# Kernel tuning notes

Measured on AMD Instinct MI355X. Metric: run time of the kernel, lower is better.

## Reference

```python
import jax, jax.numpy as jnp
import numpy as np


def setup_inputs() -> dict:
    key = jax.random.key(0)
    k1, k2, k3 = jax.random.split(key, 3)
    B, N, D = 8, 4096, 64
    q = jax.random.normal(k1, (B, N, D), dtype=jnp.float32)
    k = jax.random.normal(k2, (B, N, D), dtype=jnp.float32)
    v = jax.random.normal(k3, (B, N, D), dtype=jnp.float32)
    attn_mask = jnp.ones((B, N), dtype=jnp.int32)  # 1 = attend, 0 = padding
    return {"q": q, "k": k, "v": v, "attn_mask": attn_mask}


def reference(q, k, v, attn_mask):
    # q: [B, n_q, d], k/v: [B, n_k, d], attn_mask: [B, n_k]
    d = q.shape[-1]
    n_q, n_k = q.shape[1], k.shape[1]
    scale = jnp.sqrt(jnp.asarray(d, dtype=q.dtype))
    # [B, n_q, n_k] attention logits
    logits = jnp.einsum("bqd,bkd->bqk", q, k) / scale
    # causal (mask_future=True): tril keep-mask over (n_q, n_k)
    causal = jnp.tril(jnp.ones((n_q, n_k), dtype=bool))
    neg_inf = jnp.asarray(-jnp.inf, dtype=logits.dtype)
    logits = jnp.where(causal[None, :, :], logits, neg_inf)
    # padding mask broadcast over query dim: [B, 1, n_k]
    logits = jnp.where(attn_mask[:, None, :] == 0, neg_inf, logits)
    w = jax.nn.softmax(logits, axis=-1)
    return jnp.einsum("bqk,bkd->bqd", w, v)
```

## Files before the change

kernel.cpp:

```cpp
#include <hip/hip_runtime.h>


#define BATCH 8
#define SEQ   4096
#define DIM   64
#define QT    64
#define NKT   (SEQ / 64)

typedef __attribute__((ext_vector_type(8))) short bf16x8;
typedef __attribute__((ext_vector_type(4))) float f32x4;
typedef __attribute__((ext_vector_type(4))) unsigned u32x4;

__device__ inline short f2bf(float f) {
    unsigned u = __builtin_bit_cast(unsigned, f);
    u += 0x7FFFu + ((u >> 16) & 1u);
    return (short)(u >> 16);
}

__device__ inline unsigned pk2bf(float a, float b) {
    unsigned ua = __builtin_bit_cast(unsigned, a) + 0x8000u;
    unsigned ub = __builtin_bit_cast(unsigned, b) + 0x8000u;
    return __builtin_amdgcn_perm(ub, ua, 0x07060302u);
}

__device__ inline float fast_exp2(float x) {
#if __has_builtin(__builtin_amdgcn_exp2f)
    return __builtin_amdgcn_exp2f(x);
#else
    return exp2f(x);
#endif
}

__device__ inline void gl_lds16(const void* g, void* l) {
    __builtin_amdgcn_global_load_lds(
        (const __attribute__((address_space(1))) void*)g,
        (__attribute__((address_space(3))) void*)l, 16, 0, 0);
}

__global__ __launch_bounds__(256)
void prep_kv(const float* __restrict__ kg, const float* __restrict__ vg,
             const int* __restrict__ mg, short* __restrict__ kw,
             short* __restrict__ vw, float* __restrict__ mf) {
    const int tile = blockIdx.x;
    const float* kp = kg + (size_t)tile * 64 * DIM;
    const float* vp = vg + (size_t)tile * 64 * DIM;
    short* ko = kw + (size_t)tile * 4096;
    short* vo = vw + (size_t)tile * 4096;
    const int t = threadIdx.x;
    if (mf && t < 64) {
        const int* mp = mg + (size_t)tile * 64;
        mf[(size_t)tile * 64 + t] = mp[t] ? 0.0f : -1e30f;
    }
#pragma unroll
    for (int i = 0; i < 4; ++i) {
        const int flat = i * 256 + t;
        const int key = flat >> 4, d0 = (flat & 15) * 4;
        const float4 kv = *(const float4*)(kp + (size_t)key * DIM + d0);
        uint2 kpk;
        kpk.x = pk2bf(kv.x, kv.y); kpk.y = pk2bf(kv.z, kv.w);
        *(uint2*)(ko + (((d0 >> 3) << 6) + key) * 8 + (d0 & 7)) = kpk;
        const float4 vv = *(const float4*)(vp + (size_t)key * DIM + d0);
        const int vcell = ((key >> 5) << 2) | ((key >> 2) & 3);
        const int vj    = (((key >> 4) & 1) << 2) | (key & 3);
        vo[((vcell << 6) + d0 + 0) * 8 + vj] = f2bf(vv.x);
        vo[((vcell << 6) + d0 + 1) * 8 + vj] = f2bf(vv.y);
        vo[((vcell << 6) + d0 + 2) * 8 + vj] = f2bf(vv.z);
        vo[((vcell << 6) + d0 + 3) * 8 + vj] = f2bf(vv.w);
    }
}

__global__ __launch_bounds__(512, 6)
void attn_split3(const float* __restrict__ qg, float* __restrict__ og,
                 const short* __restrict__ kw, const short* __restrict__ vw,
                 const float* __restrict__ mf, float* __restrict__ opart,
                 float* __restrict__ lpart) {
    __shared__ __align__(16) char smem[32768];
    short* KbS = (short*)smem;
    short* VbS = (short*)(smem + 16384);
    float* OX = (float*)smem;
    float* LB = (float*)(smem + 16384);

    const int t    = threadIdx.x;
    const int w    = t >> 6;
    const int L    = t & 63;
    const int c15  = L & 15;
    const int quad = L >> 4;
    const int qsub = w & 3;
    const int kh   = w >> 2;

    const int id  = blockIdx.x;
    const int b   = id & 7;
    const int r_  = id >> 3;
    const int j   = r_ & 31;
    const int ch  = r_ >> 5;
    const int nL  = 64 - j;
    const int qLt = 63 - j;

    const float* qp  = qg + (size_t)b * SEQ * DIM;
    const float* mb  = mf + (size_t)b * SEQ;
    const short* kwb = kw + (size_t)b * NKT * 4096;
    const short* vwb = vw + (size_t)b * NKT * 4096;
    float* osl = opart + (size_t)(b * 32 + j) * 8192;
    float* lsl = lpart + (size_t)(b * 32 + j) * 256;
    const float qscale = 0.125f * 1.44269504088896340736f;

    auto stage = [&](int bs, int kt) {
        const short* ks = kwb + (size_t)kt * 4096;
        const short* vs = vwb + (size_t)kt * 4096;
        const int off = w << 9;
        gl_lds16(ks + off + (L << 3), KbS + bs * 4096 + off);
        gl_lds16(vs + off + (L << 3), VbS + bs * 4096 + off);
    };

    int sqt[2], sk0[2], sk1[2], smode[2], sos[2], sls[2], nseg;
    sos[0] = sos[1] = 0; sls[0] = sls[1] = 0;
    if (ch == 0) {
        nseg = 1;
        sqt[0] = qLt; sk0[0] = 0;  sk1[0] = 22; smode[0] = 0; sls[0] = 0;
    } else if (ch == 1) {
        if (nL >= 44) {
            nseg = 1;
            sqt[0] = qLt; sk0[0] = 22; sk1[0] = 44; smode[0] = 1; sos[0] = 0; sls[0] = 1;
        } else {
            nseg = 2;
            sqt[0] = qLt; sk0[0] = 22; sk1[0] = nL;      smode[0] = 1; sos[0] = 0; sls[0] = 1;
            sqt[1] = j;   sk0[1] = 0;  sk1[1] = 44 - nL; smode[1] = 0; sls[1] = 3;
        }
    } else {
        if (nL > 44) {
            nseg = 2;
            sqt[0] = qLt; sk0[0] = 44; sk1[0] = nL;    smode[0] = 1; sos[0] = 1; sls[0] = 2;
            sqt[1] = j;   sk0[1] = 0;  sk1[1] = j + 1; smode[1] = 2;
        } else if (nL == 44) {
            nseg = 1;
            sqt[0] = j; sk0[0] = 0; sk1[0] = j + 1; smode[0] = 2;
        } else {
            nseg = 1;
            sqt[0] = j; sk0[0] = 44 - nL; sk1[0] = j + 1; smode[0] = 1; sos[0] = 1; sls[0] = 2;
        }
    }

    for (int seg = 0; seg < nseg; ++seg) {
        const int qt   = sqt[seg];
        const int kt0  = sk0[seg];
        const int kt1  = sk1[seg];
        const int mode = smode[seg];

        const int qbase = qt * QT;
        const int qrow  = qbase + qsub * 16 + c15;

        bf16x8 Qf[2];
#pragma unroll
        for (int c = 0; c < 2; ++c) {
            const float* src = qp + (size_t)qrow * DIM + c * 32 + quad * 8;
            float4 x = *(const float4*)(src);
            float4 y = *(const float4*)(src + 4);
            bf16x8 f;
            f[0] = f2bf(x.x * qscale); f[1] = f2bf(x.y * qscale);
            f[2] = f2bf(x.z * qscale); f[3] = f2bf(x.w * qscale);
            f[4] = f2bf(y.x * qscale); f[5] = f2bf(y.y * qscale);
            f[6] = f2bf(y.z * qscale); f[7] = f2bf(y.w * qscale);
            Qf[c] = f;
        }

        float lsum = 0.0f;
        f32x4 Oacc[4];
#pragma unroll
        for (int nb = 0; nb < 4; ++nb) Oacc[nb] = (f32x4){0.f, 0.f, 0.f, 0.f};

        stage(0, kt0);

        for (int kt = kt0; kt < kt1; ++kt) {
            const int cur = (kt - kt0) & 1;
            __syncthreads();
            if (kt + 1 < kt1) stage(cur ^ 1, kt + 1);

            const short* Kt = KbS + cur * 4096;
            const short* Vt = VbS + cur * 4096;

            const float4 ma0 = *(const float4*)&mb[kt * 64 + (2 * kh + 0) * 16 + quad * 4];
            const float4 ma1 = *(const float4*)&mb[kt * 64 + (2 * kh + 1) * 16 + quad * 4];

            f32x4 sacc[2];
            sacc[0] = (f32x4){0.f, 0.f, 0.f, 0.f};
            sacc[1] = (f32x4){0.f, 0.f, 0.f, 0.f};
#pragma unroll
            for (int c = 0; c < 2; ++c) {
#pragma unroll
                for (int i = 0; i < 2; ++i) {
                    bf16x8 kf = *(const bf16x8*)&Kt[(((quad + 4 * c) << 6) + (2 * kh + i) * 16 + c15) * 8];
                    sacc[i] = __builtin_amdgcn_mfma_f32_16x16x32_bf16(kf, Qf[c], sacc[i], 0, 0, 0);
                }
            }

            const bool diag = (kt == qt);
            unsigned pu[4];
#pragma unroll
            for (int i = 0; i < 2; ++i) {
                const int kb = 2 * kh + i;
                const float4 ma = i ? ma1 : ma0;
                const float mar[4] = {ma.x, ma.y, ma.z, ma.w};
                float p[4];
#pragma unroll
                for (int r = 0; r < 4; ++r) {
                    float s = sacc[i][r] + mar[r];
                    if (diag) {
                        const int keyg = kt * 64 + kb * 16 + quad * 4 + r;
                        if (keyg > qrow) s = -1e30f;
                    }
                    p[r] = fast_exp2(fminf(s, 80.0f));
                    lsum += p[r];
                }
                pu[2 * i]     = pk2bf(p[0], p[1]);
                pu[2 * i + 1] = pk2bf(p[2], p[3]);
            }

            const bf16x8 pf = __builtin_bit_cast(bf16x8,
                (u32x4){pu[0], pu[1], pu[2], pu[3]});
#pragma unroll
            for (int nb = 0; nb < 4; ++nb) {
                bf16x8 vf = *(const bf16x8*)&Vt[(((kh * 4 + quad) << 6) + nb * 16 + c15) * 8];
                Oacc[nb] = __builtin_amdgcn_mfma_f32_16x16x32_bf16(pf, vf, Oacc[nb], 0, 0, 0);
            }
        }

        lsum += __shfl_xor(lsum, 16);
        lsum += __shfl_xor(lsum, 32);

        __syncthreads();
        if (w >= 4) {
            const int g = w & 3;
#pragma unroll
            for (int r = 0; r < 4; ++r) {
                const int q = quad * 4 + r;
#pragma unroll
                for (int nb = 0; nb < 4; ++nb)
                    OX[(g * 16 + q) * 64 + nb * 16 + c15] = Oacc[nb][r];
            }
            if (quad == 0) LB[g * 16 + c15] = lsum;
        }
        __syncthreads();
        if (w < 4) {
            const float ltot = lsum + LB[w * 16 + c15];
            const float inv  = 1.0f / ltot;
            float* dst = (mode == 1) ? osl + (size_t)sos[seg] * 4096
                                     : og + ((size_t)b * SEQ + qbase) * DIM;
            if (mode != 2 && L < 16)
                lsl[sls[seg] * 64 + w * 16 + L] = ltot;
#pragma unroll
            for (int r = 0; r < 4; ++r) {
                const float ir = (mode == 2)
                    ? __shfl(inv, (L & 48) + ((L & 48) >> 2) + r) : 1.0f;
                const int rl = w * 16 + quad * 4 + r;
#pragma unroll
                for (int nb = 0; nb < 4; ++nb)
                    dst[(size_t)rl * DIM + nb * 16 + c15] =
                        (Oacc[nb][r] + OX[rl * 64 + nb * 16 + c15]) * ir;
            }
        }
        __syncthreads();
    }
}

__global__ __launch_bounds__(256)
void merge3(float* __restrict__ og, const float* __restrict__ opart,
            const float* __restrict__ lpart) {
    const int id = blockIdx.x;
    const int b = id & 7, j = id >> 3;
    const int nL = 64 - j, qLt = 63 - j;
    const float* os = opart + (size_t)(b * 32 + j) * 8192;
    const float* ls = lpart + (size_t)(b * 32 + j) * 256;
    const int t = threadIdx.x;
    const bool hasC = (nL > 44);

    float* opL = og + ((size_t)b * SEQ + (size_t)qLt * 64) * DIM;
#pragma unroll
    for (int i = 0; i < 4; ++i) {
        const int flat = i * 256 + t;
        const int row = flat >> 4;
        const int c4  = (flat & 15) * 4;
        float l = ls[row] + ls[64 + row];
        if (hasC) l += ls[128 + row];
        const float inv = 1.0f / l;
        const float4 a  = *(const float4*)(opL + (size_t)row * DIM + c4);
        const float4 p0 = *(const float4*)(os + (size_t)row * 64 + c4);
        float4 r;
        if (hasC) {
            const float4 p1 = *(const float4*)(os + 4096 + (size_t)row * 64 + c4);
            r.x = (a.x + p0.x + p1.x) * inv;
            r.y = (a.y + p0.y + p1.y) * inv;
            r.z = (a.z + p0.z + p1.z) * inv;
            r.w = (a.w + p0.w + p1.w) * inv;
        } else {
            r.x = (a.x + p0.x) * inv;
            r.y = (a.y + p0.y) * inv;
            r.z = (a.z + p0.z) * inv;
            r.w = (a.w + p0.w) * inv;
        }
        *(float4*)(opL + (size_t)row * DIM + c4) = r;
    }

    if (nL < 44) {
        float* opS = og + ((size_t)b * SEQ + (size_t)j * 64) * DIM;
#pragma unroll
        for (int i = 0; i < 4; ++i) {
            const int flat = i * 256 + t;
            const int row = flat >> 4;
            const int c4  = (flat & 15) * 4;
            const float inv = 1.0f / (ls[192 + row] + ls[128 + row]);
            const float4 a  = *(const float4*)(opS + (size_t)row * DIM + c4);
            const float4 p1 = *(const float4*)(os + 4096 + (size_t)row * 64 + c4);
            float4 r;
            r.x = (a.x + p1.x) * inv;
            r.y = (a.y + p1.y) * inv;
            r.z = (a.z + p1.z) * inv;
            r.w = (a.w + p1.w) * inv;
            *(float4*)(opS + (size_t)row * DIM + c4) = r;
        }
    }
}

template <bool WS>
__global__ __launch_bounds__(512, 4)
void attn_fwd(const float* __restrict__ qg, const float* __restrict__ kg,
              const float* __restrict__ vg, const int* __restrict__ mg,
              float* __restrict__ og, const short* __restrict__ kw,
              const short* __restrict__ vw) {
    __shared__ __align__(16) char smem[59392];
    short* KbS = (short*)smem;
    short* VbS = (short*)(smem + 16384);
    float* Ml  = (float*)(smem + 43008);
    float* OX = (float*)smem;
    float* LB = (float*)(smem + 16384);

    const int t    = threadIdx.x;
    const int w    = t >> 6;
    const int L    = t & 63;
    const int c15  = L & 15;
    const int quad = L >> 4;
    const int qsub = w & 3;
    const int kh   = w >> 2;

    const int id = blockIdx.x;
    const int b  = id & 7;
    const int j  = id >> 3;
    const int qb = (j < 32) ? (63 - j) : (j - 32);
    const int qbase  = qb * QT;
    const int ntiles = qb + 1;

    const float* qp = qg + (size_t)b * SEQ * DIM;
    const float* kp = kg + (size_t)b * SEQ * DIM;
    const float* vp = vg + (size_t)b * SEQ * DIM;
    const int*   mp = mg + (size_t)b * SEQ;
    const short* kwb = WS ? kw + (size_t)b * NKT * 4096 : nullptr;
    const short* vwb = WS ? vw + (size_t)b * NKT * 4096 : nullptr;

    const int qrow = qbase + qsub * 16 + c15;
    const float qscale = 0.125f * 1.44269504088896340736f;

    bf16x8 Qf[2];
#pragma unroll
    for (int c = 0; c < 2; ++c) {
        const float* src = qp + (size_t)qrow * DIM + c * 32 + quad * 8;
        float4 x = *(const float4*)(src);
        float4 y = *(const float4*)(src + 4);
        bf16x8 f;
        f[0] = f2bf(x.x * qscale); f[1] = f2bf(x.y * qscale);
        f[2] = f2bf(x.z * qscale); f[3] = f2bf(x.w * qscale);
        f[4] = f2bf(y.x * qscale); f[5] = f2bf(y.y * qscale);
        f[6] = f2bf(y.z * qscale); f[7] = f2bf(y.w * qscale);
        Qf[c] = f;
    }

    auto stage = [&](int bs, int kt) {
        const short* ks = kwb + (size_t)kt * 4096;
        const short* vs = vwb + (size_t)kt * 4096;
        const int off = w << 9;
        gl_lds16(ks + off + (L << 3), KbS + bs * 4096 + off);
        gl_lds16(vs + off + (L << 3), VbS + bs * 4096 + off);
    };

    for (int i = t; i < ntiles * 64; i += 512)
        Ml[i] = mp[i] ? 0.0f : -1e30f;

    float lsum = 0.0f;
    f32x4 Oacc[4];
#pragma unroll
    for (int nb = 0; nb < 4; ++nb) Oacc[nb] = (f32x4){0.f, 0.f, 0.f, 0.f};

    if constexpr (WS) stage(0, 0);

    for (int kt = 0; kt < ntiles; ++kt) {
        const int cur = WS ? (kt & 1) : 0;

        if constexpr (!WS) {
            __syncthreads();
#pragma unroll
            for (int it = 0; it < 2; ++it) {
                const int flat = it * 512 + t;
                const int key = flat >> 4, d0 = (flat & 15) * 4;
                const float4 kv = *(const float4*)(kp + (size_t)(kt * 64 + key) * DIM + d0);
                uint2 kk;
                kk.x = pk2bf(kv.x, kv.y); kk.y = pk2bf(kv.z, kv.w);
                *(uint2*)&KbS[(((d0 >> 3) << 6) + key) * 8 + (d0 & 7)] = kk;
                const float4 vv = *(const float4*)(vp + (size_t)(kt * 64 + key) * DIM + d0);
                const int vcell = ((key >> 5) << 2) | ((key >> 2) & 3);
                const int vj    = (((key >> 4) & 1) << 2) | (key & 3);
                VbS[((vcell << 6) + d0 + 0) * 8 + vj] = f2bf(vv.x);
                VbS[((vcell << 6) + d0 + 1) * 8 + vj] = f2bf(vv.y);
                VbS[((vcell << 6) + d0 + 2) * 8 + vj] = f2bf(vv.z);
                VbS[((vcell << 6) + d0 + 3) * 8 + vj] = f2bf(vv.w);
            }
            __syncthreads();
        } else {
            __syncthreads();
            if (kt + 1 < ntiles) stage(cur ^ 1, kt + 1);
        }

        const short* Kt = KbS + cur * 4096;
        const short* Vt = VbS + cur * 4096;

        f32x4 sacc[2];
        sacc[0] = (f32x4){0.f, 0.f, 0.f, 0.f};
        sacc[1] = (f32x4){0.f, 0.f, 0.f, 0.f};
#pragma unroll
        for (int c = 0; c < 2; ++c) {
#pragma unroll
            for (int i = 0; i < 2; ++i) {
                bf16x8 kf = *(const bf16x8*)&Kt[(((quad + 4 * c) << 6) + (2 * kh + i) * 16 + c15) * 8];
                sacc[i] = __builtin_amdgcn_mfma_f32_16x16x32_bf16(kf, Qf[c], sacc[i], 0, 0, 0);
            }
        }

        const bool diag = (kt == ntiles - 1);
        unsigned pu[4];
#pragma unroll
        for (int i = 0; i < 2; ++i) {
            const int kb = 2 * kh + i;
            const float4 ma = *(const float4*)&Ml[kt * 64 + kb * 16 + quad * 4];
            const float mar[4] = {ma.x, ma.y, ma.z, ma.w};
            float p[4];
#pragma unroll
            for (int r = 0; r < 4; ++r) {
                float s = sacc[i][r] + mar[r];
                if (diag) {
                    const int keyg = kt * 64 + kb * 16 + quad * 4 + r;
                    if (keyg > qrow) s = -1e30f;
                }
                p[r] = fast_exp2(fminf(s, 80.0f));
                lsum += p[r];
            }
            pu[2 * i]     = pk2bf(p[0], p[1]);
            pu[2 * i + 1] = pk2bf(p[2], p[3]);
        }

        const bf16x8 pf = __builtin_bit_cast(bf16x8,
            (u32x4){pu[0], pu[1], pu[2], pu[3]});
#pragma unroll
        for (int nb = 0; nb < 4; ++nb) {
            bf16x8 vf = *(const bf16x8*)&Vt[(((kh * 4 + quad) << 6) + nb * 16 + c15) * 8];
            Oacc[nb] = __builtin_amdgcn_mfma_f32_16x16x32_bf16(pf, vf, Oacc[nb], 0, 0, 0);
        }
    }

    lsum += __shfl_xor(lsum, 16);
    lsum += __shfl_xor(lsum, 32);

    __syncthreads();
    if (w >= 4) {
        const int g = w & 3;
#pragma unroll
        for (int r = 0; r < 4; ++r) {
            const int q = quad * 4 + r;
#pragma unroll
            for (int nb = 0; nb < 4; ++nb)
                OX[(g * 16 + q) * 64 + nb * 16 + c15] = Oacc[nb][r];
        }
        if (quad == 0) LB[g * 16 + c15] = lsum;
    }
    __syncthreads();
    if (w < 4) {
        const float inv = 1.0f / (lsum + LB[w * 16 + c15]);
        float* op = og + (size_t)b * SEQ * DIM;
#pragma unroll
        for (int r = 0; r < 4; ++r) {
            const float ir = __shfl(inv, (L & 48) + ((L & 48) >> 2) + r);
            const int row = qbase + w * 16 + quad * 4 + r;
#pragma unroll
            for (int nb = 0; nb < 4; ++nb)
                op[(size_t)row * DIM + nb * 16 + c15] =
                    (Oacc[nb][r] + OX[(w * 16 + quad * 4 + r) * 64 + nb * 16 + c15]) * ir;
        }
    }
}

extern "C" void kernel_launch(void* const* d_in, const int* in_sizes, int n_in,
                              void* d_out, int out_size, void* d_ws, size_t ws_size,
                              hipStream_t stream) {
    (void)in_sizes; (void)n_in; (void)out_size;
    const float* q = (const float*)d_in[0];
    const float* k = (const float*)d_in[1];
    const float* v = (const float*)d_in[2];
    const int*   m = (const int*)d_in[3];
    float* o = (float*)d_out;

    const size_t kvB    = (size_t)BATCH * NKT * 4096 * sizeof(short);
    const size_t maddB  = (size_t)BATCH * SEQ * sizeof(float);
    const size_t opartB = (size_t)BATCH * 32 * 8192 * sizeof(float);
    const size_t lpartB = (size_t)BATCH * 32 * 256 * sizeof(float);
    const size_t need3  = 2 * kvB + maddB + opartB + lpartB;

    if (ws_size >= need3) {
        short* kw = (short*)d_ws;
        short* vw = kw + (size_t)BATCH * NKT * 4096;
        float* mf = (float*)((char*)d_ws + 2 * kvB);
        float* opart = (float*)((char*)d_ws + 2 * kvB + maddB);
        float* lpart = opart + (size_t)BATCH * 32 * 8192;
        prep_kv<<<dim3(BATCH * NKT), 256, 0, stream>>>(k, v, m, kw, vw, mf);
        attn_split3<<<dim3(768), 512, 0, stream>>>(q, o, kw, vw, mf, opart, lpart);
        merge3<<<dim3(256), 256, 0, stream>>>(o, opart, lpart);
    } else if (ws_size >= 2 * kvB) {
        short* kw = (short*)d_ws;
        short* vw = kw + (size_t)BATCH * NKT * 4096;
        prep_kv<<<dim3(BATCH * NKT), 256, 0, stream>>>(k, v, m, kw, vw, nullptr);
        attn_fwd<true><<<dim3(512), 512, 0, stream>>>(q, k, v, m, o, kw, vw);
    } else {
        attn_fwd<false><<<dim3(512), 512, 0, stream>>>(q, k, v, m, o, nullptr, nullptr);
    }
}
```

Measured before the change: 124.9 us.

## Triple-buffer K/V staging with explicit vmcnt waits and MFMA row sums

Moves K/V staging from a double buffer to a triple buffer in a larger LDS allocation, prefetching two tiles ahead. The full __syncthreads at the top of each iteration becomes an explicit vmcnt wait plus a raw barrier, so loads can stay in flight longer. The softmax row sum is now produced by an extra MFMA against a vector of bf16 ones, replacing per-lane adds and the cross-lane shuffles, and the clamp before exp2 is dropped. K and V are read with nontemporal loads in the prep kernel. The costs are 48KB of LDS per block, which may reduce occupancy under the 6-block launch bound, and dropping the clamp risks overflow on large logits.

```diff
diff --git a/kernel.cpp b/kernel.cpp
--- a/kernel.cpp
+++ b/kernel.cpp
@@ -35,6 +35,10 @@
     __builtin_amdgcn_global_load_lds(
         (const __attribute__((address_space(1))) void*)g,
         (__attribute__((address_space(3))) void*)l, 16, 0, 0);
+}
+
+__device__ inline f32x4 ntl4(const float* p) {
+    return __builtin_nontemporal_load((const f32x4*)p);
 }
 
 __global__ __launch_bounds__(256)
@@ -55,17 +59,17 @@
     for (int i = 0; i < 4; ++i) {
         const int flat = i * 256 + t;
         const int key = flat >> 4, d0 = (flat & 15) * 4;
-        const float4 kv = *(const float4*)(kp + (size_t)key * DIM + d0);
+        const f32x4 kv = ntl4(kp + (size_t)key * DIM + d0);
         uint2 kpk;
-        kpk.x = pk2bf(kv.x, kv.y); kpk.y = pk2bf(kv.z, kv.w);
+        kpk.x = pk2bf(kv[0], kv[1]); kpk.y = pk2bf(kv[2], kv[3]);
         *(uint2*)(ko + (((d0 >> 3) << 6) + key) * 8 + (d0 & 7)) = kpk;
-        const float4 vv = *(const float4*)(vp + (size_t)key * DIM + d0);
+        const f32x4 vv = ntl4(vp + (size_t)key * DIM + d0);
         const int vcell = ((key >> 5) << 2) | ((key >> 2) & 3);
         const int vj    = (((key >> 4) & 1) << 2) | (key & 3);
-        vo[((vcell << 6) + d0 + 0) * 8 + vj] = f2bf(vv.x);
-        vo[((vcell << 6) + d0 + 1) * 8 + vj] = f2bf(vv.y);
-        vo[((vcell << 6) + d0 + 2) * 8 + vj] = f2bf(vv.z);
-        vo[((vcell << 6) + d0 + 3) * 8 + vj] = f2bf(vv.w);
+        vo[((vcell << 6) + d0 + 0) * 8 + vj] = f2bf(vv[0]);
+        vo[((vcell << 6) + d0 + 1) * 8 + vj] = f2bf(vv[1]);
+        vo[((vcell << 6) + d0 + 2) * 8 + vj] = f2bf(vv[2]);
+        vo[((vcell << 6) + d0 + 3) * 8 + vj] = f2bf(vv[3]);
     }
 }
 
@@ -74,9 +78,8 @@
                  const short* __restrict__ kw, const short* __restrict__ vw,
                  const float* __restrict__ mf, float* __restrict__ opart,
                  float* __restrict__ lpart) {
-    __shared__ __align__(16) char smem[32768];
+    __shared__ __align__(16) char smem[49152];
     short* KbS = (short*)smem;
-    short* VbS = (short*)(smem + 16384);
     float* OX = (float*)smem;
     float* LB = (float*)(smem + 16384);
 
@@ -108,9 +111,13 @@
         const short* ks = kwb + (size_t)kt * 4096;
         const short* vs = vwb + (size_t)kt * 4096;
         const int off = w << 9;
-        gl_lds16(ks + off + (L << 3), KbS + bs * 4096 + off);
-        gl_lds16(vs + off + (L << 3), VbS + bs * 4096 + off);
+        gl_lds16(ks + off + (L << 3), KbS + bs * 8192 + off);
+        gl_lds16(vs + off + (L << 3), KbS + bs * 8192 + 4096 + off);
     };
+
+    bf16x8 vones;
+#pragma unroll
+    for (int z = 0; z < 8; ++z) vones[z] = (short)0x3F80;
 
     int sqt[2], sk0[2], sk1[2], smode[2], sos[2], sls[2], nseg;
     sos[0] = sos[1] = 0; sls[0] = sls[1] = 0;
@@ -162,24 +169,34 @@
             f[6] = f2bf(y.z * qscale); f[7] = f2bf(y.w * qscale);
             Qf[c] = f;
         }
-
-        float lsum = 0.0f;
+        asm volatile("" ::: "memory");
+
+        f32x4 lacc = (f32x4){0.f, 0.f, 0.f, 0.f};
         f32x4 Oacc[4];
 #pragma unroll
         for (int nb = 0; nb < 4; ++nb) Oacc[nb] = (f32x4){0.f, 0.f, 0.f, 0.f};
 
         stage(0, kt0);
+        if (kt0 + 1 < kt1) stage(1, kt0 + 1);
 
         for (int kt = kt0; kt < kt1; ++kt) {
-            const int cur = (kt - kt0) & 1;
-            __syncthreads();
-            if (kt + 1 < kt1) stage(cur ^ 1, kt + 1);
-
-            const short* Kt = KbS + cur * 4096;
-            const short* Vt = VbS + cur * 4096;
+            const int bi = (kt - kt0) % 3;
+
+            if (kt + 1 < kt1) {
+                asm volatile("s_waitcnt vmcnt(2)" ::: "memory");
+            } else {
+                asm volatile("s_waitcnt vmcnt(0)" ::: "memory");
+            }
+            __builtin_amdgcn_s_barrier();
+            asm volatile("" ::: "memory");
 
             const float4 ma0 = *(const float4*)&mb[kt * 64 + (2 * kh + 0) * 16 + quad * 4];
             const float4 ma1 = *(const float4*)&mb[kt * 64 + (2 * kh + 1) * 16 + quad * 4];
+            asm volatile("" ::: "memory");
+            if (kt + 2 < kt1) stage((kt + 2 - kt0) % 3, kt + 2);
+
+            const short* Kt = KbS + bi * 8192;
+            const short* Vt = Kt + 4096;
 
             f32x4 sacc[2];
             sacc[0] = (f32x4){0.f, 0.f, 0.f, 0.f};
@@ -208,8 +225,7 @@
                         const int keyg = kt * 64 + kb * 16 + quad * 4 + r;
                         if (keyg > qrow) s = -1e30f;
                     }
-                    p[r] = fast_exp2(fminf(s, 80.0f));
-                    lsum += p[r];
+                    p[r] = fast_exp2(s);
                 }
                 pu[2 * i]     = pk2bf(p[0], p[1]);
                 pu[2 * i + 1] = pk2bf(p[2], p[3]);
@@ -222,10 +238,8 @@
                 bf16x8 vf = *(const bf16x8*)&Vt[(((kh * 4 + quad) << 6) + nb * 16 + c15) * 8];
                 Oacc[nb] = __builtin_amdgcn_mfma_f32_16x16x32_bf16(pf, vf, Oacc[nb], 0, 0, 0);
             }
-        }
-
-        lsum += __shfl_xor(lsum, 16);
-        lsum += __shfl_xor(lsum, 32);
+            lacc = __builtin_amdgcn_mfma_f32_16x16x32_bf16(pf, vones, lacc, 0, 0, 0);
+        }
 
         __syncthreads();
         if (w >= 4) {
@@ -237,20 +251,30 @@
                 for (int nb = 0; nb < 4; ++nb)
                     OX[(g * 16 + q) * 64 + nb * 16 + c15] = Oacc[nb][r];
             }
-            if (quad == 0) LB[g * 16 + c15] = lsum;
+            if (c15 == 0) {
+#pragma unroll
+                for (int r = 0; r < 4; ++r)
+                    LB[g * 16 + quad * 4 + r] = lacc[r];
+            }
         }
         __syncthreads();
         if (w < 4) {
-            const float ltot = lsum + LB[w * 16 + c15];
-            const float inv  = 1.0f / ltot;
+            float lt_[4], inv_[4];
+#pragma unroll
+            for (int r = 0; r < 4; ++r) {
+                lt_[r]  = lacc[r] + LB[w * 16 + quad * 4 + r];
+                inv_[r] = 1.0f / lt_[r];
+            }
             float* dst = (mode == 1) ? osl + (size_t)sos[seg] * 4096
                                      : og + ((size_t)b * SEQ + qbase) * DIM;
-            if (mode != 2 && L < 16)
-                lsl[sls[seg] * 64 + w * 16 + L] = ltot;
+            if (mode != 2 && c15 == 0) {
+#pragma unroll
+                for (int r = 0; r < 4; ++r)
+                    lsl[sls[seg] * 64 + w * 16 + quad * 4 + r] = lt_[r];
+            }
 #pragma unroll
             for (int r = 0; r < 4; ++r) {
-                const float ir = (mode == 2)
-                    ? __shfl(inv, (L & 48) + ((L & 48) >> 2) + r) : 1.0f;
+                const float ir = (mode == 2) ? inv_[r] : 1.0f;
                 const int rl = w * 16 + quad * 4 + r;
 #pragma unroll
                 for (int nb = 0; nb < 4; ++nb)
```

After: 120.3 us. 3.7% less time.
